# Optimization experiments

Hardware: AMD Instinct MI355X
Metric: run time of the kernel (lower is better)

The kernel has to match this reference:

```python
import jax, jax.numpy as jnp
import numpy as np

N_NODES = 65536
N_GRAPHS = 1024
NODES_PER_G = 64
N_EDGES = 1048576
IN_FEATS = 512
HIDDEN = 1024
H4 = 256
EMB = 512
EPS = 1e-5
SLOPE = 0.01


def setup_inputs() -> dict:
    key = jax.random.key(0)
    ks = jax.random.split(key, 10)
    # within-graph random edges: edge e belongs to graph e // (E/B)
    epg = N_EDGES // N_GRAPHS
    eg = np.arange(N_EDGES) // epg
    rng = np.random.default_rng(0)
    src = rng.integers(0, NODES_PER_G, N_EDGES) + eg * NODES_PER_G
    dst = rng.integers(0, NODES_PER_G, N_EDGES) + eg * NODES_PER_G
    node_gid = np.arange(N_NODES) // NODES_PER_G
    return {
        "node_feats": jax.random.normal(ks[0], (N_NODES, IN_FEATS), jnp.float32),
        "edge_weights": jax.random.uniform(ks[1], (N_EDGES,), jnp.float32),
        "W1": jax.random.normal(ks[2], (IN_FEATS, HIDDEN), jnp.float32) * 0.05,
        "W2": jax.random.normal(ks[3], (HIDDEN, H4), jnp.float32) * 0.05,
        "W_emb": jax.random.normal(ks[4], (IN_FEATS + HIDDEN + H4, EMB), jnp.float32) * 0.02,
        "gn1_alpha": jnp.ones((HIDDEN,), jnp.float32),
        "gn1_gamma": jnp.ones((HIDDEN,), jnp.float32),
        "gn1_beta": jnp.zeros((HIDDEN,), jnp.float32),
        "gn2_alpha": jnp.ones((H4,), jnp.float32),
        "gn2_gamma": jnp.ones((H4,), jnp.float32),
        "gn2_beta": jnp.zeros((H4,), jnp.float32),
        "edge_src": jnp.asarray(src, jnp.int32),
        "edge_dst": jnp.asarray(dst, jnp.int32),
        "node_gid": jnp.asarray(node_gid, jnp.int32),
    }


def _seg_sum(x, ids, num):
    return jax.ops.segment_sum(x, ids, num_segments=num)


def _graph_conv(x, W, src, dst, ew):
    # DGL GraphConv, norm='both', bias=False, with edge_weight (u_mul_e)
    ones = jnp.ones((src.shape[0],), x.dtype)
    deg_out = jnp.clip(_seg_sum(ones, src, N_NODES), 1.0)
    deg_in = jnp.clip(_seg_sum(ones, dst, N_NODES), 1.0)
    h = (x * jax.lax.rsqrt(deg_out)[:, None]) @ W
    msg = h[src] * ew[:, None]
    agg = _seg_sum(msg, dst, N_NODES)
    return agg * jax.lax.rsqrt(deg_in)[:, None]


def _graph_norm(x, gid, counts, alpha, gamma, beta):
    # GraphNorm (Cai et al.): learnable mean-scale alpha, per-graph stats
    mean = _seg_sum(x, gid, N_GRAPHS) / counts[:, None]
    sub = x - alpha * mean[gid]
    var = _seg_sum(sub * sub, gid, N_GRAPHS) / counts[:, None]
    return gamma * sub * jax.lax.rsqrt(var[gid] + EPS) + beta


def _mean_nodes(x, gid, counts):
    return _seg_sum(x, gid, N_GRAPHS) / counts[:, None]


def _leaky(x):
    return jnp.where(x >= 0, x, SLOPE * x)


def reference(node_feats, edge_weights, W1, W2, W_emb,
              gn1_alpha, gn1_gamma, gn1_beta,
              gn2_alpha, gn2_gamma, gn2_beta,
              edge_src, edge_dst, node_gid):
    counts = jnp.clip(_seg_sum(jnp.ones((N_NODES,), node_feats.dtype), node_gid, N_GRAPHS), 1.0)
    r0 = _mean_nodes(node_feats, node_gid, counts)                 # [B, in]
    h1 = _graph_conv(node_feats, W1, edge_src, edge_dst, edge_weights)
    h1 = _leaky(_graph_norm(h1, node_gid, counts, gn1_alpha, gn1_gamma, gn1_beta))
    r1 = _mean_nodes(h1, node_gid, counts)                          # [B, hidden]
    h2 = _graph_conv(h1, W2, edge_src, edge_dst, edge_weights)
    h2 = _leaky(_graph_norm(h2, node_gid, counts, gn2_alpha, gn2_gamma, gn2_beta))
    r2 = _mean_nodes(h2, node_gid, counts)                          # [B, hidden/4]
    emb = jnp.concatenate([r0, r1, r2], axis=1) @ W_emb             # [B, EMB]
    # InstanceNorm1d on [B, E] input: per-row normalization, no affine
    mu = jnp.mean(emb, axis=1, keepdims=True)
    var = jnp.mean((emb - mu) ** 2, axis=1, keepdims=True)
    emb = (emb - mu) * jax.lax.rsqrt(var + EPS)
    return _leaky(emb)
```

## Files before the change

kernel.cpp:

```cpp
#include <hip/hip_runtime.h>
#include <hip/hip_bf16.h>
#include <stdint.h>

#define N_NODES   65536
#define N_GRAPHS  1024
#define N_EDGES   1048576
#define IN_FEATS  512
#define HIDDEN    1024
#define H4        256
#define EMB_DIM   512
#define RDIM      1792
#define EPS_F     1e-5f
#define SLOPE_F   0.01f

typedef __bf16 bf16;
typedef __bf16 bf16x4 __attribute__((ext_vector_type(4)));
typedef __bf16 bf16x8 __attribute__((ext_vector_type(8)));
typedef float  floatx4 __attribute__((ext_vector_type(4)));

#define GLDS16(gp, lp) __builtin_amdgcn_global_load_lds( \
    (const __attribute__((address_space(1))) void*)(gp), \
    (__attribute__((address_space(3))) void*)(lp), 16, 0, 0)

__global__ __launch_bounds__(256) void k_graph_build(
    const int* __restrict__ src, const int* __restrict__ dst,
    const float* __restrict__ ew,
    bf16* __restrict__ adjb, float* __restrict__ scl_o)
{
    __shared__ float sAdj[4096];
    __shared__ float sDegO[64], sDegI[64];
    int g = blockIdx.x, tid = threadIdx.x;
    for (int i = tid; i < 4096; i += 256) sAdj[i] = 0.f;
    if (tid < 64) { sDegO[tid] = 0.f; sDegI[tid] = 0.f; }
    __syncthreads();
    int e0 = g * 1024;
    #pragma unroll
    for (int i = 0; i < 4; ++i) {
        int e = e0 + i * 256 + tid;
        int s = src[e] & 63, d = dst[e] & 63;
        atomicAdd(&sAdj[(d << 6) | s], ew[e]);
        atomicAdd(&sDegO[s], 1.f);
        atomicAdd(&sDegI[d], 1.f);
    }
    __syncthreads();
    if (tid < 64) scl_o[g * 64 + tid] = rsqrtf(fmaxf(sDegO[tid], 1.f));
    bf16* ag = adjb + ((size_t)g << 12);
    for (int i = tid; i < 4096; i += 256) {
        float si = rsqrtf(fmaxf(sDegI[i >> 6], 1.f));
        ag[i] = (bf16)(sAdj[i] * si);
    }
}

__global__ __launch_bounds__(256) void k_transpose_t(
    const float* __restrict__ W, bf16* __restrict__ WT, int K, int N)
{
    __shared__ float sT[64][65];
    const int k0 = blockIdx.x * 64, n0 = blockIdx.y * 64;
    const int tid = threadIdx.x;
    const int lr = tid >> 4, lc = (tid & 15) * 4;
    #pragma unroll
    for (int i = 0; i < 4; ++i) {
        int row = lr + i * 16;
        float4 v = *(const float4*)&W[(size_t)(k0 + row) * N + n0 + lc];
        sT[row][lc + 0] = v.x; sT[row][lc + 1] = v.y;
        sT[row][lc + 2] = v.z; sT[row][lc + 3] = v.w;
    }
    __syncthreads();
    const int nn = tid >> 2, kk0 = (tid & 3) * 16;
    #pragma unroll
    for (int h = 0; h < 2; ++h) {
        bf16x8 o;
        #pragma unroll
        for (int j = 0; j < 8; ++j)
            o[j] = (bf16)sT[kk0 + h * 8 + j][nn];
        *(bf16x8*)&WT[(size_t)(n0 + nn) * K + k0 + kk0 + h * 8] = o;
    }
}

__global__ __launch_bounds__(256) void k_prep_agg1(
    const float* __restrict__ x, const float* __restrict__ so,
    const bf16* __restrict__ adjb,
    bf16* __restrict__ axs1, bf16* __restrict__ Rb)
{
    __shared__ __align__(16) bf16 sXrT[256 * 64];
    __shared__ __align__(16) bf16 sOut[64 * 264];
    __shared__ float sSo[64];
    int g = blockIdx.x >> 1, half = blockIdx.x & 1;
    int tid = threadIdx.x, lane = tid & 63, wave = tid >> 6, q = lane >> 4;
    if (tid < 64) sSo[tid] = so[g * 64 + tid];

    const float* xg = x + (size_t)g * 64 * IN_FEATS + half * 256;
    const bf16* ag = adjb + ((size_t)g << 12);

    bf16x8 af[4][2];
    #pragma unroll
    for (int mt = 0; mt < 4; ++mt)
        #pragma unroll
        for (int kk = 0; kk < 2; ++kk)
            af[mt][kk] = *(const bf16x8*)&ag[(mt * 16 + (lane & 15)) * 64 + kk * 32 + q * 8];
    __syncthreads();

    float r0 = 0.f;
    const int sw = tid & 7;
    #pragma unroll
    for (int r8 = 0; r8 < 8; ++r8) {
        bf16x8 p;
        #pragma unroll
        for (int j = 0; j < 8; ++j) {
            int r = r8 * 8 + j;
            float v = xg[(size_t)r * IN_FEATS + tid];
            r0 += v;
            p[j] = (bf16)(v * sSo[r]);
        }
        *(bf16x8*)&sXrT[tid * 64 + ((r8 ^ sw) * 8)] = p;
    }
    Rb[(size_t)g * RDIM + half * 256 + tid] = (bf16)(r0 * (1.f / 64.f));
    __syncthreads();

    #pragma unroll
    for (int nt = 0; nt < 4; ++nt) {
        int cl = wave * 64 + nt * 16 + (lane & 15);
        floatx4 acc[4] = {};
        #pragma unroll
        for (int kk = 0; kk < 2; ++kk) {
            bf16x8 bfrag = *(const bf16x8*)&sXrT[cl * 64 + (((kk * 4 + q) ^ (cl & 7)) * 8)];
            #pragma unroll
            for (int mt = 0; mt < 4; ++mt)
                acc[mt] = __builtin_amdgcn_mfma_f32_16x16x32_bf16(af[mt][kk], bfrag, acc[mt], 0, 0, 0);
        }
        #pragma unroll
        for (int mt = 0; mt < 4; ++mt)
            #pragma unroll
            for (int i = 0; i < 4; ++i)
                sOut[(mt * 16 + q * 4 + i) * 264 + cl] = (bf16)acc[mt][i];
    }
    __syncthreads();
    #pragma unroll
    for (int it = 0; it < 8; ++it) {
        int idx = it * 256 + tid;
        int d = idx >> 5, c8 = idx & 31;
        *(bf16x8*)&axs1[(size_t)(g * 64 + d) * IN_FEATS + half * 256 + c8 * 8] =
            *(const bf16x8*)&sOut[d * 264 + c8 * 8];
    }
}

__global__ __launch_bounds__(512) void k_gemm12(
    const bf16* __restrict__ A, const bf16* __restrict__ BT1,
    const bf16* __restrict__ BT2, const bf16* __restrict__ adjb,
    const float* __restrict__ al1, const float* __restrict__ ga1, const float* __restrict__ be1,
    const float* __restrict__ al2, const float* __restrict__ ga2, const float* __restrict__ be2,
    const float* __restrict__ so, bf16* __restrict__ Rb)
{
    __shared__ __align__(16) bf16 sm[66560];
    __shared__ float sSo[128];
    const int tid = threadIdx.x;
    const int lane = tid & 63, wave = tid >> 6, q = lane >> 4;
    const int wm = wave >> 2, wn = wave & 3;
    const int by = blockIdx.x;
    const int row0 = by * 128;
    const int gw = by * 2 + wm;
    if (tid < 128) sSo[tid] = so[row0 + tid];

    floatx4 acc2[4][4] = {};
    bf16* sX = sm + 49152;

    #pragma unroll 1
    for (int ct = 0; ct < 8; ++ct) {
        floatx4 acc1[4][2] = {};

        auto stage_ab = [&](int k0, int buf) {
            #pragma unroll
            for (int ro = 0; ro < 2; ++ro) {
                int u = ro * 4096 + wave * 512 + lane * 8;
                int r = u >> 6, c = ((u >> 3) & 7) ^ (r & 7);
                GLDS16(A   + (size_t)(row0 + r) * IN_FEATS + k0 + c * 8,
                       sm + buf * 16384 + ro * 4096 + wave * 512);
                GLDS16(BT1 + (size_t)(ct * 128 + r) * IN_FEATS + k0 + c * 8,
                       sm + buf * 16384 + 8192 + ro * 4096 + wave * 512);
            }
        };
        auto stage_w2 = [&](int h, int buf) {
            #pragma unroll
            for (int ro = 0; ro < 4; ++ro) {
                int u = ro * 4096 + wave * 512 + lane * 8;
                int r = u >> 6, c = ((u >> 3) & 7) ^ (r & 7);
                GLDS16(BT2 + (size_t)r * HIDDEN + ct * 128 + h * 64 + c * 8,
                       sm + buf * 16384 + ro * 4096 + wave * 512);
            }
        };
        auto mfma_step = [&](int buf) {
            const bf16* sA = sm + buf * 16384;
            const bf16* sB = sA + 8192;
            #pragma unroll
            for (int kk = 0; kk < 2; ++kk) {
                bf16x8 afr[4], bfr[2];
                int cw = kk * 4 + q;
                #pragma unroll
                for (int mt = 0; mt < 4; ++mt) {
                    int r = wm * 64 + mt * 16 + (lane & 15);
                    afr[mt] = *(const bf16x8*)&sA[(r * 8 + (cw ^ (r & 7))) * 8];
                }
                #pragma unroll
                for (int nt = 0; nt < 2; ++nt) {
                    int r = wn * 32 + nt * 16 + (lane & 15);
                    bfr[nt] = *(const bf16x8*)&sB[(r * 8 + (cw ^ (r & 7))) * 8];
                }
                #pragma unroll
                for (int mt = 0; mt < 4; ++mt)
                    #pragma unroll
                    for (int nt = 0; nt < 2; ++nt)
                        acc1[mt][nt] = __builtin_amdgcn_mfma_f32_16x16x32_bf16(
                            afr[mt], bfr[nt], acc1[mt][nt], 0, 0, 0);
            }
        };

        stage_ab(0, 0);
        stage_ab(64, 1);

        #pragma unroll
        for (int t = 0; t < 8; ++t) {
            asm volatile("s_waitcnt vmcnt(4)" ::: "memory");
            __builtin_amdgcn_s_barrier();
            if (t < 6)       stage_ab((t + 2) * 64, (t + 2) % 3);
            else if (t == 6) stage_w2(0, 2);
            else             stage_w2(1, 0);
            mfma_step(t % 3);
        }

        #pragma unroll
        for (int nt = 0; nt < 2; ++nt) {
            int cl = wn * 32 + nt * 16 + (lane & 15);
            int colg = ct * 128 + cl;
            float lsum = 0.f;
            #pragma unroll
            for (int mt = 0; mt < 4; ++mt)
                #pragma unroll
                for (int i = 0; i < 4; ++i) lsum += acc1[mt][nt][i];
            lsum += __shfl_xor(lsum, 16);
            lsum += __shfl_xor(lsum, 32);
            float am = al1[colg] * (lsum * (1.f / 64.f));
            float gm = ga1[colg], bt = be1[colg];
            float sub[4][4], qv = 0.f;
            #pragma unroll
            for (int mt = 0; mt < 4; ++mt)
                #pragma unroll
                for (int i = 0; i < 4; ++i) {
                    float d = acc1[mt][nt][i] - am;
                    sub[mt][i] = d; qv += d * d;
                }
            qv += __shfl_xor(qv, 16);
            qv += __shfl_xor(qv, 32);
            float rs = rsqrtf(qv * (1.f / 64.f) + EPS_F);
            float rsum = 0.f;
            #pragma unroll
            for (int mt = 0; mt < 4; ++mt)
                #pragma unroll
                for (int i = 0; i < 4; ++i) {
                    float o = gm * sub[mt][i] * rs + bt;
                    o = (o >= 0.f) ? o : SLOPE_F * o;
                    rsum += o;
                    int r = wm * 64 + mt * 16 + q * 4 + i;
                    sX[r * 136 + cl] = (bf16)(o * sSo[r]);
                }
            rsum += __shfl_xor(rsum, 16);
            rsum += __shfl_xor(rsum, 32);
            if (lane < 16)
                Rb[(size_t)gw * RDIM + 512 + colg] = (bf16)(rsum * (1.f / 64.f));
        }
        asm volatile("s_waitcnt vmcnt(0)" ::: "memory");
        __syncthreads();

        #pragma unroll
        for (int kk2 = 0; kk2 < 4; ++kk2) {
            const bf16* sW = sm + ((kk2 < 2) ? 2 : 0) * 16384;
            int cw = (kk2 & 1) * 4 + q;
            bf16x8 afr[4], bfr[4];
            #pragma unroll
            for (int mt = 0; mt < 4; ++mt)
                afr[mt] = *(const bf16x8*)&sX[(wm * 64 + mt * 16 + (lane & 15)) * 136 + kk2 * 32 + q * 8];
            #pragma unroll
            for (int nt = 0; nt < 4; ++nt) {
                int r = wn * 64 + nt * 16 + (lane & 15);
                bfr[nt] = *(const bf16x8*)&sW[(r * 8 + (cw ^ (r & 7))) * 8];
            }
            #pragma unroll
            for (int mt = 0; mt < 4; ++mt)
                #pragma unroll
                for (int nt = 0; nt < 4; ++nt)
                    acc2[mt][nt] = __builtin_amdgcn_mfma_f32_16x16x32_bf16(
                        afr[mt], bfr[nt], acc2[mt][nt], 0, 0, 0);
        }
        __syncthreads();
    }

    bf16* sT = sm;
    #pragma unroll
    for (int nt = 0; nt < 4; ++nt) {
        int cl = wn * 64 + nt * 16 + (lane & 15);
        #pragma unroll
        for (int mt = 0; mt < 4; ++mt)
            #pragma unroll
            for (int i = 0; i < 4; ++i)
                sT[cl * 136 + wm * 64 + mt * 16 + q * 4 + i] = (bf16)acc2[mt][nt][i];
    }
    asm volatile("s_waitcnt lgkmcnt(0)" ::: "memory");

    const bf16* ag = adjb + ((size_t)gw << 12);
    floatx4 hh[4][4] = {};
    #pragma unroll
    for (int kk = 0; kk < 2; ++kk) {
        bf16x8 afr[4], bfr[4];
        #pragma unroll
        for (int mt = 0; mt < 4; ++mt)
            afr[mt] = *(const bf16x8*)&ag[(mt * 16 + (lane & 15)) * 64 + kk * 32 + q * 8];
        #pragma unroll
        for (int nt = 0; nt < 4; ++nt)
            bfr[nt] = *(const bf16x8*)&sT[(wn * 64 + nt * 16 + (lane & 15)) * 136 + wm * 64 + kk * 32 + q * 8];
        #pragma unroll
        for (int mt = 0; mt < 4; ++mt)
            #pragma unroll
            for (int nt = 0; nt < 4; ++nt)
                hh[mt][nt] = __builtin_amdgcn_mfma_f32_16x16x32_bf16(afr[mt], bfr[nt], hh[mt][nt], 0, 0, 0);
    }

    #pragma unroll
    for (int nt = 0; nt < 4; ++nt) {
        int colg = wn * 64 + nt * 16 + (lane & 15);
        float lsum = 0.f;
        #pragma unroll
        for (int mt = 0; mt < 4; ++mt)
            #pragma unroll
            for (int i = 0; i < 4; ++i) lsum += hh[mt][nt][i];
        lsum += __shfl_xor(lsum, 16);
        lsum += __shfl_xor(lsum, 32);
        float am = al2[colg] * (lsum * (1.f / 64.f));
        float gm = ga2[colg], bt = be2[colg];
        float sub[4][4], qv = 0.f;
        #pragma unroll
        for (int mt = 0; mt < 4; ++mt)
            #pragma unroll
            for (int i = 0; i < 4; ++i) {
                float d = hh[mt][nt][i] - am;
                sub[mt][i] = d; qv += d * d;
            }
        qv += __shfl_xor(qv, 16);
        qv += __shfl_xor(qv, 32);
        float rs = rsqrtf(qv * (1.f / 64.f) + EPS_F);
        float rsum = 0.f;
        #pragma unroll
        for (int mt = 0; mt < 4; ++mt)
            #pragma unroll
            for (int i = 0; i < 4; ++i) {
                float o = gm * sub[mt][i] * rs + bt;
                rsum += (o >= 0.f) ? o : SLOPE_F * o;
            }
        rsum += __shfl_xor(rsum, 16);
        rsum += __shfl_xor(rsum, 32);
        if (lane < 16)
            Rb[(size_t)gw * RDIM + 1536 + colg] = (bf16)(rsum * (1.f / 64.f));
    }
}

__device__ __forceinline__ void swizzle_block(int cb, int& bx, int& by)
{
    int b = blockIdx.y * gridDim.x + blockIdx.x;
    int xcd = b & 7, t = b >> 3;
    bx = t % cb;
    by = (t / cb) * 8 + xcd;
}

__global__ __launch_bounds__(256) void k_gemm_ro(
    const bf16* __restrict__ A, const bf16* __restrict__ BT,
    float* __restrict__ Cout)
{
    __shared__ __align__(16) bf16 sm[65536];
    const int tid = threadIdx.x;
    const int lane = tid & 63, wave = tid >> 6, q = lane >> 4;
    const int wm = wave & 1, wn = wave >> 1;
    int bx, by; swizzle_block(gridDim.x, bx, by);
    const int row0 = by * 128, col0 = bx * 128;

    floatx4 acc[4][4] = {};

    auto stage = [&](int k0, int buf) {
        #pragma unroll
        for (int i = 0; i < 4; ++i) {
            int u = (wave * 4 + i) * 64 + lane;
            int r = u >> 3, c = (u & 7) ^ (r & 7);
            GLDS16(A  + (size_t)(row0 + r) * RDIM + (k0 + c * 8),
                   sm + buf * 16384 + (wave * 4 + i) * 512);
            GLDS16(BT + (size_t)(col0 + r) * RDIM + (k0 + c * 8),
                   sm + buf * 16384 + 8192 + (wave * 4 + i) * 512);
        }
    };
    auto step = [&](int buf) {
        const bf16* sA = sm + buf * 16384;
        const bf16* sB = sA + 8192;
        #pragma unroll
        for (int kk = 0; kk < 2; ++kk) {
            bf16x8 afr[4], bfr[4];
            int cw = kk * 4 + q;
            #pragma unroll
            for (int mt = 0; mt < 4; ++mt) {
                int r = wm * 64 + mt * 16 + (lane & 15);
                afr[mt] = *(const bf16x8*)&sA[(r * 8 + (cw ^ (r & 7))) * 8];
            }
            #pragma unroll
            for (int nt = 0; nt < 4; ++nt) {
                int r = wn * 64 + nt * 16 + (lane & 15);
                bfr[nt] = *(const bf16x8*)&sB[(r * 8 + (cw ^ (r & 7))) * 8];
            }
            #pragma unroll
            for (int mt = 0; mt < 4; ++mt)
                #pragma unroll
                for (int nt = 0; nt < 4; ++nt)
                    acc[mt][nt] = __builtin_amdgcn_mfma_f32_16x16x32_bf16(
                        afr[mt], bfr[nt], acc[mt][nt], 0, 0, 0);
        }
    };

    stage(0, 0); stage(64, 1); stage(128, 2);
    #pragma unroll 1
    for (int t = 0; t < 26; ++t) {
        asm volatile("s_waitcnt vmcnt(16)" ::: "memory");
        __builtin_amdgcn_s_barrier();
        if (t < 25) stage((t + 3) * 64, (t + 3) & 3);
        step(t & 3);
    }
    asm volatile("s_waitcnt vmcnt(8)" ::: "memory");
    __builtin_amdgcn_s_barrier();
    step(2);
    asm volatile("s_waitcnt vmcnt(0)" ::: "memory");
    __builtin_amdgcn_s_barrier();
    step(3);

    #pragma unroll
    for (int mt = 0; mt < 4; ++mt)
        #pragma unroll
        for (int nt = 0; nt < 4; ++nt) {
            int col = col0 + wn * 64 + nt * 16 + (lane & 15);
            #pragma unroll
            for (int i = 0; i < 4; ++i) {
                int row = row0 + wm * 64 + mt * 16 + q * 4 + i;
                Cout[(size_t)row * EMB_DIM + col] = acc[mt][nt][i];
            }
        }
}

__global__ __launch_bounds__(256) void k_instnorm(
    const float* __restrict__ emb, float* __restrict__ out)
{
    int row = blockIdx.x, tid = threadIdx.x;
    int lane = tid & 63, wave = tid >> 6;
    __shared__ float sS[4], sQ[4];
    float v0 = emb[(size_t)row * EMB_DIM + tid];
    float v1 = emb[(size_t)row * EMB_DIM + 256 + tid];
    float s = v0 + v1, q = v0 * v0 + v1 * v1;
    #pragma unroll
    for (int off = 32; off; off >>= 1) {
        s += __shfl_down(s, off);
        q += __shfl_down(q, off);
    }
    if (lane == 0) { sS[wave] = s; sQ[wave] = q; }
    __syncthreads();
    float S = sS[0] + sS[1] + sS[2] + sS[3];
    float Q = sQ[0] + sQ[1] + sQ[2] + sQ[3];
    float mu = S * (1.f / 512.f);
    float var = Q * (1.f / 512.f) - mu * mu;
    float rs = rsqrtf(var + EPS_F);
    float o0 = (v0 - mu) * rs; o0 = (o0 >= 0.f) ? o0 : SLOPE_F * o0;
    float o1 = (v1 - mu) * rs; o1 = (o1 >= 0.f) ? o1 : SLOPE_F * o1;
    out[(size_t)row * EMB_DIM + tid]       = o0;
    out[(size_t)row * EMB_DIM + 256 + tid] = o1;
}

extern "C" void kernel_launch(void* const* d_in, const int* in_sizes, int n_in,
                              void* d_out, int out_size, void* d_ws, size_t ws_size,
                              hipStream_t stream) {
    const float* x    = (const float*)d_in[0];
    const float* ew   = (const float*)d_in[1];
    const float* W1   = (const float*)d_in[2];
    const float* W2   = (const float*)d_in[3];
    const float* Wemb = (const float*)d_in[4];
    const float* a1   = (const float*)d_in[5];
    const float* g1   = (const float*)d_in[6];
    const float* b1   = (const float*)d_in[7];
    const float* a2   = (const float*)d_in[8];
    const float* g2   = (const float*)d_in[9];
    const float* b2   = (const float*)d_in[10];
    const int* esrc   = (const int*)d_in[11];
    const int* edst   = (const int*)d_in[12];
    float* out = (float*)d_out;

    char* ws = (char*)d_ws;
    const size_t MB = 1024ull * 1024ull;
    bf16*  adjb   = (bf16*)(ws);
    float* scl_o  = (float*)(ws + 8 * MB);
    bf16*  Rb     = (bf16*)(ws + 9 * MB);
    bf16*  W1T    = (bf16*)(ws + 13 * MB);
    bf16*  W2T    = (bf16*)(ws + 14 * MB);
    bf16*  WembT  = (bf16*)(ws + 15 * MB);
    float* emb    = (float*)(ws + 17 * MB);
    bf16*  axs1   = (bf16*)(ws + 20 * MB);

    k_graph_build<<<N_GRAPHS, 256, 0, stream>>>(esrc, edst, ew, adjb, scl_o);
    k_transpose_t<<<dim3(IN_FEATS / 64, HIDDEN / 64), 256, 0, stream>>>(W1, W1T, IN_FEATS, HIDDEN);
    k_transpose_t<<<dim3(HIDDEN / 64, H4 / 64), 256, 0, stream>>>(W2, W2T, HIDDEN, H4);
    k_transpose_t<<<dim3(RDIM / 64, EMB_DIM / 64), 256, 0, stream>>>(Wemb, WembT, RDIM, EMB_DIM);

    k_prep_agg1<<<N_GRAPHS * 2, 256, 0, stream>>>(x, scl_o, adjb, axs1, Rb);

    k_gemm12<<<N_NODES / 128, 512, 0, stream>>>(
        axs1, W1T, W2T, adjb, a1, g1, b1, a2, g2, b2, scl_o, Rb);

    k_gemm_ro<<<dim3(EMB_DIM / 128, N_GRAPHS / 128), 256, 0, stream>>>(
        Rb, WembT, emb);
    k_instnorm<<<N_GRAPHS, 256, 0, stream>>>(emb, out);

    (void)in_sizes; (void)n_in; (void)out_size; (void)ws_size;
}
```

Baseline: 422.0 us.

## Shrink gemm12 LDS footprint with K=32 stages and merge weight transposes

The fused GEMM kernel now stages A/W1 tiles in 32-wide K chunks (16 steps instead of 8) and loads W2 in two halves into a single buffer. This cuts shared memory from about 133KB to about 82KB, which could allow more blocks per CU or better latency hiding. The deg_out scaling moves from the sX writes (via an LDS array) to the acc2 epilogue (loaded from global), which is algebraically equivalent. The three weight-transpose launches are merged into one launch. In exchange there are more barriers per tile, and the W2 load is less overlapped with the GraphNorm epilogue.

Result: no change. 428.1 us (+1.4%).

```diff
diff --git a/kernel.cpp b/kernel.cpp
--- a/kernel.cpp
+++ b/kernel.cpp
@@ -51,11 +51,18 @@
     }
 }
 
-__global__ __launch_bounds__(256) void k_transpose_t(
-    const float* __restrict__ W, bf16* __restrict__ WT, int K, int N)
+__global__ __launch_bounds__(256) void k_transpose3(
+    const float* __restrict__ W1, bf16* __restrict__ W1T,
+    const float* __restrict__ W2, bf16* __restrict__ W2T,
+    const float* __restrict__ We, bf16* __restrict__ WeT)
 {
     __shared__ float sT[64][65];
-    const int k0 = blockIdx.x * 64, n0 = blockIdx.y * 64;
+    int b = blockIdx.x;
+    const float* W; bf16* WT; int K, N, bx, by;
+    if (b < 128)      { W = W1; WT = W1T; K = 512;  N = 1024; bx = b & 7;  by = b >> 3; }
+    else if (b < 192) { b -= 128; W = W2; WT = W2T; K = 1024; N = 256;  bx = b & 15; by = b >> 4; }
+    else              { b -= 192; W = We; WT = WeT; K = 1792; N = 512;  bx = b % 28; by = b / 28; }
+    const int k0 = bx * 64, n0 = by * 64;
     const int tid = threadIdx.x;
     const int lr = tid >> 4, lc = (tid & 15) * 4;
     #pragma unroll
@@ -151,81 +158,79 @@
     const float* __restrict__ al2, const float* __restrict__ ga2, const float* __restrict__ be2,
     const float* __restrict__ so, bf16* __restrict__ Rb)
 {
-    __shared__ __align__(16) bf16 sm[66560];
-    __shared__ float sSo[128];
+    __shared__ __align__(16) bf16 sm[40960];
     const int tid = threadIdx.x;
     const int lane = tid & 63, wave = tid >> 6, q = lane >> 4;
     const int wm = wave >> 2, wn = wave & 3;
     const int by = blockIdx.x;
     const int row0 = by * 128;
     const int gw = by * 2 + wm;
-    if (tid < 128) sSo[tid] = so[row0 + tid];
 
     floatx4 acc2[4][4] = {};
-    bf16* sX = sm + 49152;
+    bf16* sX = sm + 24576;
+
+    auto stage_ab = [&](int k0, int buf, int ct) {
+        int u = tid * 8;
+        int r = u >> 5;
+        int cg = (u >> 3) & 3;
+        int cs = cg ^ (r & 3);
+        GLDS16(A   + (size_t)(row0 + r) * IN_FEATS + k0 + cs * 8,
+               sm + buf * 8192 + u);
+        GLDS16(BT1 + (size_t)(ct * 128 + r) * IN_FEATS + k0 + cs * 8,
+               sm + buf * 8192 + 4096 + u);
+    };
+    auto stage_w2h = [&](int ct, int h) {
+        #pragma unroll
+        for (int i = 0; i < 4; ++i) {
+            int u = i * 4096 + tid * 8;
+            int rr = u >> 6;
+            int cg = (u >> 3) & 7;
+            int cs = cg ^ (rr & 7);
+            GLDS16(BT2 + (size_t)rr * HIDDEN + ct * 128 + h * 64 + cs * 8,
+                   sm + u);
+        }
+    };
 
     #pragma unroll 1
     for (int ct = 0; ct < 8; ++ct) {
         floatx4 acc1[4][2] = {};
 
-        auto stage_ab = [&](int k0, int buf) {
-            #pragma unroll
-            for (int ro = 0; ro < 2; ++ro) {
-                int u = ro * 4096 + wave * 512 + lane * 8;
-                int r = u >> 6, c = ((u >> 3) & 7) ^ (r & 7);
-                GLDS16(A   + (size_t)(row0 + r) * IN_FEATS + k0 + c * 8,
-                       sm + buf * 16384 + ro * 4096 + wave * 512);
-                GLDS16(BT1 + (size_t)(ct * 128 + r) * IN_FEATS + k0 + c * 8,
-                       sm + buf * 16384 + 8192 + ro * 4096 + wave * 512);
-            }
+        auto mfma_step = [&](int buf) {
+            const bf16* sA = sm + buf * 8192;
+            const bf16* sB = sA + 4096;
+            bf16x8 afr[4], bfr[2];
+            #pragma unroll
+            for (int mt = 0; mt < 4; ++mt) {
+                int r = wm * 64 + mt * 16 + (lane & 15);
+                afr[mt] = *(const bf16x8*)&sA[r * 32 + ((q ^ (r & 3)) * 8)];
+            }
+            #pragma unroll
+            for (int nt = 0; nt < 2; ++nt) {
+                int r = wn * 32 + nt * 16 + (lane & 15);
+                bfr[nt] = *(const bf16x8*)&sB[r * 32 + ((q ^ (r & 3)) * 8)];
+            }
+            #pragma unroll
+            for (int mt = 0; mt < 4; ++mt)
+                #pragma unroll
+                for (int nt = 0; nt < 2; ++nt)
+                    acc1[mt][nt] = __builtin_amdgcn_mfma_f32_16x16x32_bf16(
+                        afr[mt], bfr[nt], acc1[mt][nt], 0, 0, 0);
         };
-        auto stage_w2 = [&](int h, int buf) {
-            #pragma unroll
-            for (int ro = 0; ro < 4; ++ro) {
-                int u = ro * 4096 + wave * 512 + lane * 8;
-                int r = u >> 6, c = ((u >> 3) & 7) ^ (r & 7);
-                GLDS16(BT2 + (size_t)r * HIDDEN + ct * 128 + h * 64 + c * 8,
-                       sm + buf * 16384 + ro * 4096 + wave * 512);
-            }
-        };
-        auto mfma_step = [&](int buf) {
-            const bf16* sA = sm + buf * 16384;
-            const bf16* sB = sA + 8192;
-            #pragma unroll
-            for (int kk = 0; kk < 2; ++kk) {
-                bf16x8 afr[4], bfr[2];
-                int cw = kk * 4 + q;
-                #pragma unroll
-                for (int mt = 0; mt < 4; ++mt) {
-                    int r = wm * 64 + mt * 16 + (lane & 15);
-                    afr[mt] = *(const bf16x8*)&sA[(r * 8 + (cw ^ (r & 7))) * 8];
-                }
-                #pragma unroll
-                for (int nt = 0; nt < 2; ++nt) {
-                    int r = wn * 32 + nt * 16 + (lane & 15);
-                    bfr[nt] = *(const bf16x8*)&sB[(r * 8 + (cw ^ (r & 7))) * 8];
-                }
-                #pragma unroll
-                for (int mt = 0; mt < 4; ++mt)
-                    #pragma unroll
-                    for (int nt = 0; nt < 2; ++nt)
-                        acc1[mt][nt] = __builtin_amdgcn_mfma_f32_16x16x32_bf16(
-                            afr[mt], bfr[nt], acc1[mt][nt], 0, 0, 0);
-            }
-        };
-
-        stage_ab(0, 0);
-        stage_ab(64, 1);
-
-        #pragma unroll
-        for (int t = 0; t < 8; ++t) {
-            asm volatile("s_waitcnt vmcnt(4)" ::: "memory");
+
+        stage_ab(0, 0, ct);
+        stage_ab(32, 1, ct);
+
+        #pragma unroll
+        for (int t = 0; t < 16; ++t) {
+            if (t < 15) { asm volatile("s_waitcnt vmcnt(2)" ::: "memory"); }
+            else        { asm volatile("s_waitcnt vmcnt(0)" ::: "memory"); }
             __builtin_amdgcn_s_barrier();
-            if (t < 6)       stage_ab((t + 2) * 64, (t + 2) % 3);
-            else if (t == 6) stage_w2(0, 2);
-            else             stage_w2(1, 0);
+            if (t < 14) stage_ab((t + 2) * 32, (t + 2) % 3, ct);
             mfma_step(t % 3);
         }
+        __syncthreads();
+
+        stage_w2h(ct, 0);
 
         #pragma unroll
         for (int nt = 0; nt < 2; ++nt) {
@@ -252,6 +257,7 @@
             qv += __shfl_xor(qv, 32);
             float rs = rsqrtf(qv * (1.f / 64.f) + EPS_F);
             float rsum = 0.f;
+            int cg = cl >> 3, c7 = cl & 7;
             #pragma unroll
             for (int mt = 0; mt < 4; ++mt)
                 #pragma unroll
@@ -260,7 +266,7 @@
                     o = (o >= 0.f) ? o : SLOPE_F * o;
                     rsum += o;
                     int r = wm * 64 + mt * 16 + q * 4 + i;
-                    sX[r * 136 + cl] = (bf16)(o * sSo[r]);
+                    sX[r * 128 + ((cg ^ (r & 15)) * 8 + c7)] = (bf16)o;
                 }
             rsum += __shfl_xor(rsum, 16);
             rsum += __shfl_xor(rsum, 32);
@@ -271,27 +277,44 @@
         __syncthreads();
 
         #pragma unroll
-        for (int kk2 = 0; kk2 < 4; ++kk2) {
-            const bf16* sW = sm + ((kk2 < 2) ? 2 : 0) * 16384;
-            int cw = (kk2 & 1) * 4 + q;
-            bf16x8 afr[4], bfr[4];
-            #pragma unroll
-            for (int mt = 0; mt < 4; ++mt)
-                afr[mt] = *(const bf16x8*)&sX[(wm * 64 + mt * 16 + (lane & 15)) * 136 + kk2 * 32 + q * 8];
-            #pragma unroll
-            for (int nt = 0; nt < 4; ++nt) {
-                int r = wn * 64 + nt * 16 + (lane & 15);
-                bfr[nt] = *(const bf16x8*)&sW[(r * 8 + (cw ^ (r & 7))) * 8];
-            }
-            #pragma unroll
-            for (int mt = 0; mt < 4; ++mt)
-                #pragma unroll
-                for (int nt = 0; nt < 4; ++nt)
-                    acc2[mt][nt] = __builtin_amdgcn_mfma_f32_16x16x32_bf16(
-                        afr[mt], bfr[nt], acc2[mt][nt], 0, 0, 0);
+        for (int h = 0; h < 2; ++h) {
+            if (h == 1) {
+                __builtin_amdgcn_s_barrier();
+                stage_w2h(ct, 1);
+                asm volatile("s_waitcnt vmcnt(0)" ::: "memory");
+                __builtin_amdgcn_s_barrier();
+            }
+            #pragma unroll
+            for (int kkh = 0; kkh < 2; ++kkh) {
+                int kk2 = h * 2 + kkh;
+                bf16x8 afr[4], bfr[4];
+                #pragma unroll
+                for (int mt = 0; mt < 4; ++mt) {
+                    int r = wm * 64 + mt * 16 + (lane & 15);
+                    afr[mt] = *(const bf16x8*)&sX[r * 128 + (((kk2 * 4 + q) ^ (r & 15)) * 8)];
+                }
+                #pragma unroll
+                for (int nt = 0; nt < 4; ++nt) {
+                    int r = wn * 64 + nt * 16 + (lane & 15);
+                    bfr[nt] = *(const bf16x8*)&sm[r * 64 + (((kkh * 4 + q) ^ (r & 7)) * 8)];
+                }
+                #pragma unroll
+                for (int mt = 0; mt < 4; ++mt)
+                    #pragma unroll
+                    for (int nt = 0; nt < 4; ++nt)
+                        acc2[mt][nt] = __builtin_amdgcn_mfma_f32_16x16x32_bf16(
+                            afr[mt], bfr[nt], acc2[mt][nt], 0, 0, 0);
+            }
         }
         __syncthreads();
     }
+
+    float sov[4][4];
+    #pragma unroll
+    for (int mt = 0; mt < 4; ++mt)
+        #pragma unroll
+        for (int i = 0; i < 4; ++i)
+            sov[mt][i] = so[row0 + wm * 64 + mt * 16 + q * 4 + i];
 
     bf16* sT = sm;
     #pragma unroll
@@ -301,7 +324,8 @@
         for (int mt = 0; mt < 4; ++mt)
             #pragma unroll
             for (int i = 0; i < 4; ++i)
-                sT[cl * 136 + wm * 64 + mt * 16 + q * 4 + i] = (bf16)acc2[mt][nt][i];
+                sT[cl * 136 + wm * 64 + mt * 16 + q * 4 + i] =
+                    (bf16)(acc2[mt][nt][i] * sov[mt][i]);
     }
     asm volatile("s_waitcnt lgkmcnt(0)" ::: "memory");
 
@@ -504,9 +528,7 @@
     bf16*  axs1   = (bf16*)(ws + 20 * MB);
 
     k_graph_build<<<N_GRAPHS, 256, 0, stream>>>(esrc, edst, ew, adjb, scl_o);
-    k_transpose_t<<<dim3(IN_FEATS / 64, HIDDEN / 64), 256, 0, stream>>>(W1, W1T, IN_FEATS, HIDDEN);
-    k_transpose_t<<<dim3(HIDDEN / 64, H4 / 64), 256, 0, stream>>>(W2, W2T, HIDDEN, H4);
-    k_transpose_t<<<dim3(RDIM / 64, EMB_DIM / 64), 256, 0, stream>>>(Wemb, WembT, RDIM, EMB_DIM);
+    k_transpose3<<<416, 256, 0, stream>>>(W1, W1T, W2, W2T, Wemb, WembT);
 
     k_prep_agg1<<<N_GRAPHS * 2, 256, 0, stream>>>(x, scl_o, adjb, axs1, Rb);
 
```
